# Kernel tuning notes

Hardware: AMD Instinct MI355X
Metric: run time of the kernel (lower is better)

Reference implementation:

```python
import jax, jax.numpy as jnp
import numpy as np

QMAX = 127.0          # int8 clip bound (symmetric, preserve-zero)
QDIV = 127.5          # AQT int8 scale divisor: 2**(bits-1) - 0.5


def _safe(s):
    # avoid div-by-zero for all-zero rows/cols
    return jnp.where(s == 0.0, 1.0, s)


def setup_inputs() -> dict:
    key = jax.random.key(0)
    k1, k2 = jax.random.split(key)
    lhs = jax.random.normal(k1, (8192, 4096), dtype=jnp.float32)
    rhs = jax.random.normal(k2, (4096, 4096), dtype=jnp.float32)
    return {"lhs": lhs, "rhs": rhs}


def reference(lhs, rhs):
    # --- dynamic symmetric int8 quantization (AQT abs-max calibration) ---
    # lhs: contract over axis 1 -> per-row scale [M, 1]
    s_l = _safe(jnp.max(jnp.abs(lhs), axis=1, keepdims=True) / QDIV)
    # rhs: contract over axis 0 -> per-column scale [1, N]
    s_r = _safe(jnp.max(jnp.abs(rhs), axis=0, keepdims=True) / QDIV)

    q_l = jnp.clip(jnp.round(lhs / s_l), -QMAX, QMAX).astype(jnp.int8)
    q_r = jnp.clip(jnp.round(rhs / s_r), -QMAX, QMAX).astype(jnp.int8)

    # --- integer matmul with int32 accumulation ---
    acc = jax.lax.dot_general(
        q_l, q_r,
        dimension_numbers=(((1,), (0,)), ((), ())),
        preferred_element_type=jnp.int32,
    )

    # --- dequantize: outer product of per-row / per-column scales ---
    return acc.astype(jnp.float32) * s_l * s_r
```

## Files before the change

kernel.cpp:

```cpp
#include <hip/hip_runtime.h>
#include <stdint.h>

#define M_DIM 8192
#define N_DIM 4096
#define K_DIM 4096
#define QMAXF 127.0f
#define QDIVF 127.5f

typedef int v4i __attribute__((ext_vector_type(4)));

typedef __attribute__((address_space(3))) void lds_void_t;
typedef __attribute__((address_space(1))) const void glb_void_t;

static __device__ __forceinline__ void load_lds16(const void* g, void* l) {
    __builtin_amdgcn_global_load_lds((glb_void_t*)g, (lds_void_t*)l, 16, 0, 0);
}

__global__ __launch_bounds__(256) void row_quant_kernel(
        const float* __restrict__ lhs, float* __restrict__ sL,
        int8_t* __restrict__ ql) {
    const int row = blockIdx.x;
    const float4* rp = (const float4*)(lhs + (size_t)row * K_DIM);
    const int t = threadIdx.x;
    float4 v[4];
    float m = 0.0f;
#pragma unroll
    for (int i = 0; i < 4; ++i) {
        v[i] = rp[t + i * 256];
        m = fmaxf(m, fmaxf(fmaxf(fabsf(v[i].x), fabsf(v[i].y)),
                           fmaxf(fabsf(v[i].z), fabsf(v[i].w))));
    }
#pragma unroll
    for (int off = 32; off; off >>= 1) m = fmaxf(m, __shfl_down(m, off, 64));
    __shared__ float wmax[4];
    if ((t & 63) == 0) wmax[t >> 6] = m;
    __syncthreads();
    const float mm = fmaxf(fmaxf(wmax[0], wmax[1]), fmaxf(wmax[2], wmax[3]));
    float s = mm / QDIVF;
    s = (s == 0.0f) ? 1.0f : s;
    if (t == 0) sL[row] = s;
    unsigned* qo = (unsigned*)ql + (size_t)row * 1024;
#pragma unroll
    for (int i = 0; i < 4; ++i) {
        int q0 = (int)fminf(fmaxf(rintf(v[i].x / s), -QMAXF), QMAXF);
        int q1 = (int)fminf(fmaxf(rintf(v[i].y / s), -QMAXF), QMAXF);
        int q2 = (int)fminf(fmaxf(rintf(v[i].z / s), -QMAXF), QMAXF);
        int q3 = (int)fminf(fmaxf(rintf(v[i].w / s), -QMAXF), QMAXF);
        qo[t + i * 256] = (q0 & 255) | ((q1 & 255) << 8) | ((q2 & 255) << 16)
                        | ((unsigned)(q3 & 255) << 24);
    }
}

__global__ __launch_bounds__(256) void col_absmax_kernel(
        const float* __restrict__ rhs, unsigned* __restrict__ bits) {
    const int col = blockIdx.x * 256 + threadIdx.x;
    const int r0 = blockIdx.y * 64;
    float m = 0.0f;
#pragma unroll 4
    for (int r = 0; r < 64; ++r)
        m = fmaxf(m, fabsf(rhs[(size_t)(r0 + r) * N_DIM + col]));
    atomicMax(&bits[col], __float_as_uint(m));
}

__global__ __launch_bounds__(256) void col_scale_kernel(
        const unsigned* __restrict__ bits, float* __restrict__ sR) {
    const int c = blockIdx.x * 256 + threadIdx.x;
    float s = __uint_as_float(bits[c]) / QDIVF;
    sR[c] = (s == 0.0f) ? 1.0f : s;
}

__global__ __launch_bounds__(256) void quant_rhs_t_kernel(
        const float* __restrict__ rhs, const float* __restrict__ sR,
        int8_t* __restrict__ qbT) {
    __shared__ __align__(16) int8_t lt[64][80];
    const int n0 = blockIdx.x * 64;
    const int k0 = blockIdx.y * 64;
    const int t = threadIdx.x;
    const int nloc = t & 63;
    const int kq = (t >> 6) * 16;
    const float s = sR[n0 + nloc];
#pragma unroll
    for (int i = 0; i < 4; ++i) {
        unsigned pack = 0;
#pragma unroll
        for (int j = 0; j < 4; ++j) {
            int kk = kq + i * 4 + j;
            float x = rhs[(size_t)(k0 + kk) * N_DIM + n0 + nloc];
            int q = (int)fminf(fmaxf(rintf(x / s), -QMAXF), QMAXF);
            pack |= (unsigned)(q & 255) << (8 * j);
        }
        *(unsigned*)&lt[nloc][kq + i * 4] = pack;
    }
    __syncthreads();
    const int nn = t >> 2, ch = t & 3;
    v4i val = *(const v4i*)&lt[nn][ch * 16];
    *(v4i*)&qbT[(size_t)(n0 + nn) * K_DIM + k0 + ch * 16] = val;
}


#define BAR() do { asm volatile("" ::: "memory");          \
                   __builtin_amdgcn_s_barrier();           \
                   asm volatile("" ::: "memory"); } while (0)

#define VMCNT(N) asm volatile("s_waitcnt vmcnt(%0)" :: "n"(N) : "memory")

#define STAGE_A(h, kt, bq) \
    load_lds16(gA0 + (size_t)((h) * 128) * K_DIM + (size_t)(kt) * 64, \
               lds + (bq) * 16384 + (h) * 8192 + sdst)
#define STAGE_B(h, kt, bq) \
    load_lds16(gB0 + (size_t)((h) * 128) * K_DIM + (size_t)(kt) * 64, \
               lds + 65536 + (bq) * 16384 + (h) * 8192 + sdst)

#define RD_A(BUF, MM) (*(const v4i*)(lds + (BUF) * 16384 + aoff[MM]))
#define RD_B(BUF, NN) (*(const v4i*)(lds + (BUF) * 16384 + boff[NN]))

#define TILE(KT, BUF, P, S, VM, RDN) do {                                       \
    _Pragma("unroll") for (int nn = 0; nn < 4; ++nn)                            \
        bfII[nn] = RD_B(BUF, 4 + nn);                                           \
    if (S) { STAGE_A(0, (KT) + 3, ((BUF) + 3) & 3);                             \
             STAGE_A(1, (KT) + 3, ((BUF) + 3) & 3);                             \
             STAGE_B(0, (KT) + 3, ((BUF) + 3) & 3);                             \
             STAGE_B(1, (KT) + 3, ((BUF) + 3) & 3); }                           \
    __builtin_amdgcn_s_setprio(1);                                              \
    _Pragma("unroll") for (int mm = 0; mm < 4; ++mm)                            \
    _Pragma("unroll") for (int nn = 0; nn < 4; ++nn)                            \
        acc[mm][nn] = __builtin_amdgcn_mfma_i32_16x16x64_i8(                    \
            af[P][mm], bfI[P][nn], acc[mm][nn], 0, 0, 0);                       \
    __builtin_amdgcn_s_setprio(0);                                              \
    if (RDN) {                                                                  \
        _Pragma("unroll") for (int mm = 0; mm < 4; ++mm)                        \
            af[(P) ^ 1][mm] = RD_A(((BUF) + 1) & 3, mm);                        \
        _Pragma("unroll") for (int nn = 0; nn < 4; ++nn)                        \
            bfI[(P) ^ 1][nn] = RD_B(((BUF) + 1) & 3, nn);                       \
    }                                                                           \
    __builtin_amdgcn_s_setprio(1);                                              \
    _Pragma("unroll") for (int mm = 0; mm < 4; ++mm)                            \
    _Pragma("unroll") for (int nn = 0; nn < 4; ++nn)                            \
        acc[mm][4 + nn] = __builtin_amdgcn_mfma_i32_16x16x64_i8(                \
            af[P][mm], bfII[nn], acc[mm][4 + nn], 0, 0, 0);                     \
    __builtin_amdgcn_s_setprio(0);                                              \
    VMCNT(VM);                                                                  \
    BAR();                                                                      \
} while (0)

__global__ __launch_bounds__(512, 2) void gemm_i8_kernel(
        const int8_t* __restrict__ qa, const int8_t* __restrict__ qbT,
        const float* __restrict__ sL, const float* __restrict__ sR,
        float* __restrict__ out) {
    __shared__ __align__(16) int8_t lds[131072];

    const int t = threadIdx.x;
    const int wave = t >> 6;
    const int lane = t & 63;

    const int bid = blockIdx.x;
    const int swz = (bid & 7) * 64 + (bid >> 3);
    const int brow = (swz & 31) * 256;
    const int bcol = (swz >> 5) * 256;

    const int wm = (wave >> 1) * 64;
    const int wn = (wave & 1) * 128;

    int aoff[4], boff[8];
#pragma unroll
    for (int m = 0; m < 4; ++m) {
        int row = wm + m * 16 + (lane & 15);
        aoff[m] = row * 64 + (((lane >> 4) ^ ((row >> 1) & 3)) * 16);
    }
#pragma unroll
    for (int n = 0; n < 8; ++n) {
        int row = wn + n * 16 + (lane & 15);
        boff[n] = 65536 + row * 64 + (((lane >> 4) ^ ((row >> 1) & 3)) * 16);
    }

    v4i acc[4][8];
#pragma unroll
    for (int m = 0; m < 4; ++m)
#pragma unroll
        for (int n = 0; n < 8; ++n) acc[m][n] = (v4i){0, 0, 0, 0};

    const int srow = t >> 2;
    const int lc = (t & 3) ^ ((srow >> 1) & 3);
    const int8_t* gA0 = qa  + (size_t)(brow + srow) * K_DIM + lc * 16;
    const int8_t* gB0 = qbT + (size_t)(bcol + srow) * K_DIM + lc * 16;
    const int sdst = t * 16;

    v4i af[2][4], bfI[2][4], bfII[4];

    STAGE_A(0, 0, 0); STAGE_A(1, 0, 0); STAGE_B(0, 0, 0); STAGE_B(1, 0, 0);
    STAGE_A(0, 1, 1); STAGE_A(1, 1, 1); STAGE_B(0, 1, 1); STAGE_B(1, 1, 1);
    STAGE_A(0, 2, 2); STAGE_A(1, 2, 2); STAGE_B(0, 2, 2); STAGE_B(1, 2, 2);
    VMCNT(4);
    BAR();
#pragma unroll
    for (int mm = 0; mm < 4; ++mm) af[0][mm] = RD_A(0, mm);
#pragma unroll
    for (int nn = 0; nn < 4; ++nn) bfI[0][nn] = RD_B(0, nn);

    for (int kt = 0; kt < 60; kt += 4) {
        TILE(kt + 0, 0, 0, 1, 4, 1);
        TILE(kt + 1, 1, 1, 1, 4, 1);
        TILE(kt + 2, 2, 0, 1, 4, 1);
        TILE(kt + 3, 3, 1, 1, 4, 1);
    }
    TILE(60, 0, 0, 1, 4, 1);
    TILE(61, 1, 1, 0, 0, 1);
    TILE(62, 2, 0, 0, 0, 1);
    TILE(63, 3, 1, 0, 0, 0);

    const int r4 = (lane >> 4) * 4;
    const int cc = lane & 15;
#pragma unroll
    for (int m = 0; m < 4; ++m) {
        const int grow0 = brow + wm + m * 16 + r4;
        const float s0 = sL[grow0 + 0];
        const float s1 = sL[grow0 + 1];
        const float s2 = sL[grow0 + 2];
        const float s3 = sL[grow0 + 3];
#pragma unroll
        for (int n = 0; n < 8; ++n) {
            const int gcol = bcol + wn + n * 16 + cc;
            const float sc = sR[gcol];
            float* o = out + (size_t)grow0 * N_DIM + gcol;
            o[0 * N_DIM] = (float)acc[m][n][0] * s0 * sc;
            o[1 * N_DIM] = (float)acc[m][n][1] * s1 * sc;
            o[2 * N_DIM] = (float)acc[m][n][2] * s2 * sc;
            o[3 * N_DIM] = (float)acc[m][n][3] * s3 * sc;
        }
    }
}

extern "C" void kernel_launch(void* const* d_in, const int* in_sizes, int n_in,
                              void* d_out, int out_size, void* d_ws, size_t ws_size,
                              hipStream_t stream) {
    const float* lhs = (const float*)d_in[0];
    const float* rhs = (const float*)d_in[1];
    float* out = (float*)d_out;

    uint8_t* ws = (uint8_t*)d_ws;
    int8_t* ql    = (int8_t*)ws;
    int8_t* qbT   = (int8_t*)(ws + 33554432);
    float* sL     = (float*)(ws + 50331648);
    float* sR     = (float*)(ws + 50331648 + 32768);
    unsigned* bits = (unsigned*)(ws + 50331648 + 32768 + 16384);

    hipMemsetAsync(bits, 0, N_DIM * sizeof(unsigned), stream);

    row_quant_kernel<<<M_DIM, 256, 0, stream>>>(lhs, sL, ql);
    col_absmax_kernel<<<dim3(N_DIM / 256, K_DIM / 64), 256, 0, stream>>>(rhs, bits);
    col_scale_kernel<<<N_DIM / 256, 256, 0, stream>>>(bits, sR);
    quant_rhs_t_kernel<<<dim3(N_DIM / 64, K_DIM / 64), 256, 0, stream>>>(rhs, sR, qbT);
    gemm_i8_kernel<<<dim3(M_DIM / 256 * N_DIM / 256), 512, 0, stream>>>(ql, qbT, sL, sR, out);
}
```

Before: 220.2 us.

## Switch GEMM to 32x32x32 int8 MFMA, remap tile swizzle, fuse prep kernels

The GEMM inner loop now uses 32x32x32 int8 MFMA instructions with 16-int accumulators instead of 16x16x64, and LDS fragment offsets and the epilogue change to match. Block-to-tile mapping is reorganised so each XCD covers a contiguous 8x8 group of output tiles, aiming for better L2 reuse. The row-quantisation and column abs-max kernels are merged into one launch, and the column-scale computation moves into the rhs quantisation kernel, removing two launches. The larger MFMA shape may cut LDS reads per FLOP, but it alters register pressure and instruction scheduling.

Result: no change. 219.2 us (-0.5%).

```diff
diff --git a/kernel.cpp b/kernel.cpp
--- a/kernel.cpp
+++ b/kernel.cpp
@@ -7,7 +7,8 @@
 #define QMAXF 127.0f
 #define QDIVF 127.5f
 
-typedef int v4i __attribute__((ext_vector_type(4)));
+typedef int v4i  __attribute__((ext_vector_type(4)));
+typedef int v16i __attribute__((ext_vector_type(16)));
 
 typedef __attribute__((address_space(3))) void lds_void_t;
 typedef __attribute__((address_space(1))) const void glb_void_t;
@@ -16,69 +17,66 @@
     __builtin_amdgcn_global_load_lds((glb_void_t*)g, (lds_void_t*)l, 16, 0, 0);
 }
 
-__global__ __launch_bounds__(256) void row_quant_kernel(
-        const float* __restrict__ lhs, float* __restrict__ sL,
+__global__ __launch_bounds__(256) void prep1_kernel(
+        const float* __restrict__ lhs, const float* __restrict__ rhs,
+        float* __restrict__ sL, unsigned* __restrict__ bits,
         int8_t* __restrict__ ql) {
-    const int row = blockIdx.x;
-    const float4* rp = (const float4*)(lhs + (size_t)row * K_DIM);
     const int t = threadIdx.x;
-    float4 v[4];
-    float m = 0.0f;
-#pragma unroll
-    for (int i = 0; i < 4; ++i) {
-        v[i] = rp[t + i * 256];
-        m = fmaxf(m, fmaxf(fmaxf(fabsf(v[i].x), fabsf(v[i].y)),
-                           fmaxf(fabsf(v[i].z), fabsf(v[i].w))));
-    }
-#pragma unroll
-    for (int off = 32; off; off >>= 1) m = fmaxf(m, __shfl_down(m, off, 64));
-    __shared__ float wmax[4];
-    if ((t & 63) == 0) wmax[t >> 6] = m;
-    __syncthreads();
-    const float mm = fmaxf(fmaxf(wmax[0], wmax[1]), fmaxf(wmax[2], wmax[3]));
-    float s = mm / QDIVF;
-    s = (s == 0.0f) ? 1.0f : s;
-    if (t == 0) sL[row] = s;
-    unsigned* qo = (unsigned*)ql + (size_t)row * 1024;
-#pragma unroll
-    for (int i = 0; i < 4; ++i) {
-        int q0 = (int)fminf(fmaxf(rintf(v[i].x / s), -QMAXF), QMAXF);
-        int q1 = (int)fminf(fmaxf(rintf(v[i].y / s), -QMAXF), QMAXF);
-        int q2 = (int)fminf(fmaxf(rintf(v[i].z / s), -QMAXF), QMAXF);
-        int q3 = (int)fminf(fmaxf(rintf(v[i].w / s), -QMAXF), QMAXF);
-        qo[t + i * 256] = (q0 & 255) | ((q1 & 255) << 8) | ((q2 & 255) << 16)
-                        | ((unsigned)(q3 & 255) << 24);
-    }
-}
-
-__global__ __launch_bounds__(256) void col_absmax_kernel(
-        const float* __restrict__ rhs, unsigned* __restrict__ bits) {
-    const int col = blockIdx.x * 256 + threadIdx.x;
-    const int r0 = blockIdx.y * 64;
-    float m = 0.0f;
+    if (blockIdx.x < M_DIM) {
+        const int row = blockIdx.x;
+        const float4* rp = (const float4*)(lhs + (size_t)row * K_DIM);
+        float4 v[4];
+        float m = 0.0f;
+#pragma unroll
+        for (int i = 0; i < 4; ++i) {
+            v[i] = rp[t + i * 256];
+            m = fmaxf(m, fmaxf(fmaxf(fabsf(v[i].x), fabsf(v[i].y)),
+                               fmaxf(fabsf(v[i].z), fabsf(v[i].w))));
+        }
+#pragma unroll
+        for (int off = 32; off; off >>= 1) m = fmaxf(m, __shfl_down(m, off, 64));
+        __shared__ float wmax[4];
+        if ((t & 63) == 0) wmax[t >> 6] = m;
+        __syncthreads();
+        const float mm = fmaxf(fmaxf(wmax[0], wmax[1]), fmaxf(wmax[2], wmax[3]));
+        float s = mm / QDIVF;
+        s = (s == 0.0f) ? 1.0f : s;
+        if (t == 0) sL[row] = s;
+        unsigned* qo = (unsigned*)ql + (size_t)row * 1024;
+#pragma unroll
+        for (int i = 0; i < 4; ++i) {
+            int q0 = (int)fminf(fmaxf(rintf(v[i].x / s), -QMAXF), QMAXF);
+            int q1 = (int)fminf(fmaxf(rintf(v[i].y / s), -QMAXF), QMAXF);
+            int q2 = (int)fminf(fmaxf(rintf(v[i].z / s), -QMAXF), QMAXF);
+            int q3 = (int)fminf(fmaxf(rintf(v[i].w / s), -QMAXF), QMAXF);
+            qo[t + i * 256] = (q0 & 255) | ((q1 & 255) << 8) | ((q2 & 255) << 16)
+                            | ((unsigned)(q3 & 255) << 24);
+        }
+    } else {
+        const int cb = blockIdx.x - M_DIM;
+        const int col = (cb & 15) * 256 + t;
+        const int r0 = (cb >> 4) * 64;
+        float m = 0.0f;
 #pragma unroll 4
-    for (int r = 0; r < 64; ++r)
-        m = fmaxf(m, fabsf(rhs[(size_t)(r0 + r) * N_DIM + col]));
-    atomicMax(&bits[col], __float_as_uint(m));
-}
-
-__global__ __launch_bounds__(256) void col_scale_kernel(
-        const unsigned* __restrict__ bits, float* __restrict__ sR) {
-    const int c = blockIdx.x * 256 + threadIdx.x;
-    float s = __uint_as_float(bits[c]) / QDIVF;
-    sR[c] = (s == 0.0f) ? 1.0f : s;
+        for (int r = 0; r < 64; ++r)
+            m = fmaxf(m, fabsf(rhs[(size_t)(r0 + r) * N_DIM + col]));
+        atomicMax(&bits[col], __float_as_uint(m));
+    }
 }
 
 __global__ __launch_bounds__(256) void quant_rhs_t_kernel(
-        const float* __restrict__ rhs, const float* __restrict__ sR,
-        int8_t* __restrict__ qbT) {
+        const float* __restrict__ rhs, const unsigned* __restrict__ bits,
+        float* __restrict__ sR, int8_t* __restrict__ qbT) {
     __shared__ __align__(16) int8_t lt[64][80];
     const int n0 = blockIdx.x * 64;
     const int k0 = blockIdx.y * 64;
     const int t = threadIdx.x;
     const int nloc = t & 63;
     const int kq = (t >> 6) * 16;
-    const float s = sR[n0 + nloc];
+    float s = __uint_as_float(bits[n0 + nloc]) / QDIVF;
+    s = (s == 0.0f) ? 1.0f : s;
+    if (blockIdx.y == 0 && t < 64) sR[n0 + t] = (__uint_as_float(bits[n0 + t]) / QDIVF == 0.0f)
+                                               ? 1.0f : __uint_as_float(bits[n0 + t]) / QDIVF;
 #pragma unroll
     for (int i = 0; i < 4; ++i) {
         unsigned pack = 0;
@@ -111,33 +109,33 @@
     load_lds16(gB0 + (size_t)((h) * 128) * K_DIM + (size_t)(kt) * 64, \
                lds + 65536 + (bq) * 16384 + (h) * 8192 + sdst)
 
-#define RD_A(BUF, MM) (*(const v4i*)(lds + (BUF) * 16384 + aoff[MM]))
-#define RD_B(BUF, NN) (*(const v4i*)(lds + (BUF) * 16384 + boff[NN]))
+#define RD_A(BUF, MF, KS) (*(const v4i*)(lds + (BUF) * 16384 + aoff[MF][KS]))
+#define RD_B(BUF, NF, KS) (*(const v4i*)(lds + (BUF) * 16384 + boff[NF][KS]))
 
 #define TILE(KT, BUF, P, S, VM, RDN) do {                                       \
-    _Pragma("unroll") for (int nn = 0; nn < 4; ++nn)                            \
-        bfII[nn] = RD_B(BUF, 4 + nn);                                           \
+    _Pragma("unroll") for (int mf = 0; mf < 2; ++mf) a1[mf] = RD_A(BUF, mf, 1); \
+    _Pragma("unroll") for (int nf = 0; nf < 4; ++nf) b1[nf] = RD_B(BUF, nf, 1); \
     if (S) { STAGE_A(0, (KT) + 3, ((BUF) + 3) & 3);                             \
              STAGE_A(1, (KT) + 3, ((BUF) + 3) & 3);                             \
              STAGE_B(0, (KT) + 3, ((BUF) + 3) & 3);                             \
              STAGE_B(1, (KT) + 3, ((BUF) + 3) & 3); }                           \
     __builtin_amdgcn_s_setprio(1);                                              \
-    _Pragma("unroll") for (int mm = 0; mm < 4; ++mm)                            \
-    _Pragma("unroll") for (int nn = 0; nn < 4; ++nn)                            \
-        acc[mm][nn] = __builtin_amdgcn_mfma_i32_16x16x64_i8(                    \
-            af[P][mm], bfI[P][nn], acc[mm][nn], 0, 0, 0);                       \
+    _Pragma("unroll") for (int mf = 0; mf < 2; ++mf)                            \
+    _Pragma("unroll") for (int nf = 0; nf < 4; ++nf)                            \
+        acc[mf][nf] = __builtin_amdgcn_mfma_i32_32x32x32_i8(                    \
+            a0[P][mf], b0[P][nf], acc[mf][nf], 0, 0, 0);                        \
     __builtin_amdgcn_s_setprio(0);                                              \
     if (RDN) {                                                                  \
-        _Pragma("unroll") for (int mm = 0; mm < 4; ++mm)                        \
-            af[(P) ^ 1][mm] = RD_A(((BUF) + 1) & 3, mm);                        \
-        _Pragma("unroll") for (int nn = 0; nn < 4; ++nn)                        \
-            bfI[(P) ^ 1][nn] = RD_B(((BUF) + 1) & 3, nn);                       \
+        _Pragma("unroll") for (int mf = 0; mf < 2; ++mf)                        \
+            a0[(P) ^ 1][mf] = RD_A(((BUF) + 1) & 3, mf, 0);                     \
+        _Pragma("unroll") for (int nf = 0; nf < 4; ++nf)                        \
+            b0[(P) ^ 1][nf] = RD_B(((BUF) + 1) & 3, nf, 0);                     \
     }                                                                           \
     __builtin_amdgcn_s_setprio(1);                                              \
-    _Pragma("unroll") for (int mm = 0; mm < 4; ++mm)                            \
-    _Pragma("unroll") for (int nn = 0; nn < 4; ++nn)                            \
-        acc[mm][4 + nn] = __builtin_amdgcn_mfma_i32_16x16x64_i8(                \
-            af[P][mm], bfII[nn], acc[mm][4 + nn], 0, 0, 0);                     \
+    _Pragma("unroll") for (int mf = 0; mf < 2; ++mf)                            \
+    _Pragma("unroll") for (int nf = 0; nf < 4; ++nf)                            \
+        acc[mf][nf] = __builtin_amdgcn_mfma_i32_32x32x32_i8(                    \
+            a1[mf], b1[nf], acc[mf][nf], 0, 0, 0);                              \
     __builtin_amdgcn_s_setprio(0);                                              \
     VMCNT(VM);                                                                  \
     BAR();                                                                      \
@@ -154,38 +152,45 @@
     const int lane = t & 63;
 
     const int bid = blockIdx.x;
-    const int swz = (bid & 7) * 64 + (bid >> 3);
-    const int brow = (swz & 31) * 256;
-    const int bcol = (swz >> 5) * 256;
+    const int xcd = bid & 7;
+    const int idx = bid >> 3;
+    const int mt = (xcd >> 1) * 8 + (idx & 7);
+    const int nt = (xcd & 1) * 8 + (idx >> 3);
+    const int brow = mt * 256;
+    const int bcol = nt * 256;
 
     const int wm = (wave >> 1) * 64;
     const int wn = (wave & 1) * 128;
 
-    int aoff[4], boff[8];
-#pragma unroll
-    for (int m = 0; m < 4; ++m) {
-        int row = wm + m * 16 + (lane & 15);
-        aoff[m] = row * 64 + (((lane >> 4) ^ ((row >> 1) & 3)) * 16);
-    }
-#pragma unroll
-    for (int n = 0; n < 8; ++n) {
-        int row = wn + n * 16 + (lane & 15);
-        boff[n] = 65536 + row * 64 + (((lane >> 4) ^ ((row >> 1) & 3)) * 16);
-    }
-
-    v4i acc[4][8];
-#pragma unroll
-    for (int m = 0; m < 4; ++m)
-#pragma unroll
-        for (int n = 0; n < 8; ++n) acc[m][n] = (v4i){0, 0, 0, 0};
+    int aoff[2][2], boff[4][2];
+#pragma unroll
+    for (int mf = 0; mf < 2; ++mf) {
+        int row = wm + mf * 32 + (lane & 31);
+#pragma unroll
+        for (int ks = 0; ks < 2; ++ks)
+            aoff[mf][ks] = row * 64 + (((ks * 2 + (lane >> 5)) ^ ((row >> 1) & 3)) * 16);
+    }
+#pragma unroll
+    for (int nf = 0; nf < 4; ++nf) {
+        int row = wn + nf * 32 + (lane & 31);
+#pragma unroll
+        for (int ks = 0; ks < 2; ++ks)
+            boff[nf][ks] = 65536 + row * 64 + (((ks * 2 + (lane >> 5)) ^ ((row >> 1) & 3)) * 16);
+    }
+
+    v16i acc[2][4];
+#pragma unroll
+    for (int mf = 0; mf < 2; ++mf)
+#pragma unroll
+        for (int nf = 0; nf < 4; ++nf) acc[mf][nf] = (v16i)(0);
 
     const int srow = t >> 2;
-    const int lc = (t & 3) ^ ((srow >> 1) & 3);
-    const int8_t* gA0 = qa  + (size_t)(brow + srow) * K_DIM + lc * 16;
-    const int8_t* gB0 = qbT + (size_t)(bcol + srow) * K_DIM + lc * 16;
+    const int lcA = (t & 3) ^ ((srow >> 1) & 3);
+    const int8_t* gA0 = qa  + (size_t)(brow + srow) * K_DIM + lcA * 16;
+    const int8_t* gB0 = qbT + (size_t)(bcol + srow) * K_DIM + lcA * 16;
     const int sdst = t * 16;
 
-    v4i af[2][4], bfI[2][4], bfII[4];
+    v4i a0[2][2], b0[2][4], a1[2], b1[4];
 
     STAGE_A(0, 0, 0); STAGE_A(1, 0, 0); STAGE_B(0, 0, 0); STAGE_B(1, 0, 0);
     STAGE_A(0, 1, 1); STAGE_A(1, 1, 1); STAGE_B(0, 1, 1); STAGE_B(1, 1, 1);
@@ -193,9 +198,9 @@
     VMCNT(4);
     BAR();
 #pragma unroll
-    for (int mm = 0; mm < 4; ++mm) af[0][mm] = RD_A(0, mm);
-#pragma unroll
-    for (int nn = 0; nn < 4; ++nn) bfI[0][nn] = RD_B(0, nn);
+    for (int mf = 0; mf < 2; ++mf) a0[0][mf] = RD_A(0, mf, 0);
+#pragma unroll
+    for (int nf = 0; nf < 4; ++nf) b0[0][nf] = RD_B(0, nf, 0);
 
     for (int kt = 0; kt < 60; kt += 4) {
         TILE(kt + 0, 0, 0, 1, 4, 1);
@@ -208,24 +213,29 @@
     TILE(62, 2, 0, 0, 0, 1);
     TILE(63, 3, 1, 0, 0, 0);
 
-    const int r4 = (lane >> 4) * 4;
-    const int cc = lane & 15;
-#pragma unroll
-    for (int m = 0; m < 4; ++m) {
-        const int grow0 = brow + wm + m * 16 + r4;
-        const float s0 = sL[grow0 + 0];
-        const float s1 = sL[grow0 + 1];
-        const float s2 = sL[grow0 + 2];
-        const float s3 = sL[grow0 + 3];
-#pragma unroll
-        for (int n = 0; n < 8; ++n) {
-            const int gcol = bcol + wn + n * 16 + cc;
+    const int cc = lane & 31;
+    const int lh = (lane >> 5) * 4;
+#pragma unroll
+    for (int mf = 0; mf < 2; ++mf) {
+        const int rbase = brow + wm + mf * 32 + lh;
+        float slv[16];
+#pragma unroll
+        for (int q = 0; q < 4; ++q)
+#pragma unroll
+            for (int j = 0; j < 4; ++j)
+                slv[q * 4 + j] = sL[rbase + q * 8 + j];
+#pragma unroll
+        for (int nf = 0; nf < 4; ++nf) {
+            const int gcol = bcol + wn + nf * 32 + cc;
             const float sc = sR[gcol];
-            float* o = out + (size_t)grow0 * N_DIM + gcol;
-            o[0 * N_DIM] = (float)acc[m][n][0] * s0 * sc;
-            o[1 * N_DIM] = (float)acc[m][n][1] * s1 * sc;
-            o[2 * N_DIM] = (float)acc[m][n][2] * s2 * sc;
-            o[3 * N_DIM] = (float)acc[m][n][3] * s3 * sc;
+#pragma unroll
+            for (int q = 0; q < 4; ++q)
+#pragma unroll
+                for (int j = 0; j < 4; ++j) {
+                    const int grow = rbase + q * 8 + j;
+                    out[(size_t)grow * N_DIM + gcol] =
+                        (float)acc[mf][nf][q * 4 + j] * slv[q * 4 + j] * sc;
+                }
         }
     }
 }
@@ -246,9 +256,9 @@
 
     hipMemsetAsync(bits, 0, N_DIM * sizeof(unsigned), stream);
 
-    row_quant_kernel<<<M_DIM, 256, 0, stream>>>(lhs, sL, ql);
-    col_absmax_kernel<<<dim3(N_DIM / 256, K_DIM / 64), 256, 0, stream>>>(rhs, bits);
-    col_scale_kernel<<<N_DIM / 256, 256, 0, stream>>>(bits, sR);
-    quant_rhs_t_kernel<<<dim3(N_DIM / 64, K_DIM / 64), 256, 0, stream>>>(rhs, sR, qbT);
-    gemm_i8_kernel<<<dim3(M_DIM / 256 * N_DIM / 256), 512, 0, stream>>>(ql, qbT, sL, sR, out);
-}
+    prep1_kernel<<<M_DIM + 1024, 256, 0, stream>>>(lhs, rhs, sL, bits, ql);
+    quant_rhs_t_kernel<<<dim3(N_DIM / 64, K_DIM / 64), 256, 0, stream>>>(
+        rhs, bits, sR, qbT);
+    gemm_i8_kernel<<<dim3((M_DIM / 256) * (N_DIM / 256)), 512, 0, stream>>>(
+        ql, qbT, sL, sR, out);
+}
```
